# Kernel optimization log

Hardware: AMD Instinct MI355X
Metric: run time of the kernel (lower is better)

Reference implementation:

```python
import jax, jax.numpy as jnp
import numpy as np
from jax import lax

R = 7                      # pooler_resolution
SCALES = (0.25, 0.125, 0.0625, 0.03125)
SCORE_THRESH = 0.05        # args.roi_test_score_thresh
NMS_THRESH = 0.5           # args.roi_nms_thresh
TOPK = 100                 # args.roi_nms_topk_post
SCALE_CLAMP = float(np.log(1000.0 / 16))


def _pool_level(f, boxes, scale):
    # f: [C,H,W]; boxes: [M,4] in image coords. RoIPool approximated by
    # nearest-neighbor sample at each of the 7x7 bin centers.
    C, H, W = f.shape
    b = boxes * scale
    x1, y1, x2, y2 = b[:, 0], b[:, 1], b[:, 2], b[:, 3]
    bw = jnp.maximum(x2 - x1, 1.0) / R
    bh = jnp.maximum(y2 - y1, 1.0) / R
    cs = jnp.arange(R, dtype=b.dtype) + 0.5
    gx = x1[:, None] + cs * bw[:, None]          # [M,R]
    gy = y1[:, None] + cs * bh[:, None]          # [M,R]
    ix = jnp.clip(gx.astype(jnp.int32), 0, W - 1)
    iy = jnp.clip(gy.astype(jnp.int32), 0, H - 1)
    fh = jnp.transpose(f, (1, 2, 0))             # [H,W,C]
    out = fh[iy[:, :, None], ix[:, None, :]]     # [M,R,R,C]
    return jnp.transpose(out, (0, 3, 1, 2))      # [M,C,R,R]


def _assign_levels(boxes):
    # detectron2-style FPN level assignment: canonical level 4 at size 224
    w = boxes[:, 2] - boxes[:, 0]
    h = boxes[:, 3] - boxes[:, 1]
    s = jnp.sqrt(jnp.maximum(w * h, 1e-6))
    lvl = jnp.floor(4.0 + jnp.log2(s / 224.0 + 1e-8))
    return jnp.clip(lvl, 2, 5).astype(jnp.int32) - 2   # index into p2..p5


def _pool_image(f2, f3, f4, f5, boxes):
    pooled = jnp.stack([_pool_level(f, boxes, s)
                        for f, s in zip((f2, f3, f4, f5), SCALES)])  # [4,M,C,R,R]
    idx = _assign_levels(boxes)
    return pooled[idx, jnp.arange(boxes.shape[0])]     # [M,C,R,R]


def _apply_deltas(boxes, deltas):
    w = boxes[:, 2] - boxes[:, 0]
    h = boxes[:, 3] - boxes[:, 1]
    cx = boxes[:, 0] + 0.5 * w
    cy = boxes[:, 1] + 0.5 * h
    dx, dy = deltas[:, 0], deltas[:, 1]
    dw = jnp.minimum(deltas[:, 2], SCALE_CLAMP)
    dh = jnp.minimum(deltas[:, 3], SCALE_CLAMP)
    pcx = dx * w + cx
    pcy = dy * h + cy
    pw = jnp.exp(dw) * w
    ph = jnp.exp(dh) * h
    return jnp.stack([pcx - 0.5 * pw, pcy - 0.5 * ph,
                      pcx + 0.5 * pw, pcy + 0.5 * ph], axis=1)


def _pairwise_iou(a, b):
    area_a = (a[:, 2] - a[:, 0]) * (a[:, 3] - a[:, 1])
    area_b = (b[:, 2] - b[:, 0]) * (b[:, 3] - b[:, 1])
    lt = jnp.maximum(a[:, None, :2], b[None, :, :2])
    rb = jnp.minimum(a[:, None, 2:], b[None, :, 2:])
    wh = jnp.clip(rb - lt, 0.0)
    inter = wh[..., 0] * wh[..., 1]
    return inter / jnp.maximum(area_a[:, None] + area_b[None, :] - inter, 1e-9)


def _nms_image(boxes, scores, hw):
    # boxes [M,4], scores [M], hw = (H,W) float
    H, W = hw[0], hw[1]
    boxes = jnp.stack([jnp.clip(boxes[:, 0], 0.0, W),
                       jnp.clip(boxes[:, 1], 0.0, H),
                       jnp.clip(boxes[:, 2], 0.0, W),
                       jnp.clip(boxes[:, 3], 0.0, H)], axis=1)
    order = jnp.argsort(-scores)
    b = boxes[order]
    s = scores[order]
    M = b.shape[0]
    keep0 = s > SCORE_THRESH
    iou = _pairwise_iou(b, b)
    idx = jnp.arange(M)

    def body(i, keep):
        suppress = (iou[i] > NMS_THRESH) & (idx > i) & keep[i]
        return keep & ~suppress

    keep = lax.fori_loop(0, M, body, keep0)
    keep = keep & (jnp.cumsum(keep.astype(jnp.int32)) <= TOPK)
    return b, s, keep, order


def setup_inputs() -> dict:
    key = jax.random.key(0)
    ks = jax.random.split(key, 12)
    N, M, C = 2, 1000, 256
    H, W = 800, 1216
    fc_in, fc_dim = C * R * R, 1024
    p2 = jax.random.normal(ks[0], (N, C, H // 4, W // 4), jnp.float32)
    p3 = jax.random.normal(ks[1], (N, C, H // 8, W // 8), jnp.float32)
    p4 = jax.random.normal(ks[2], (N, C, H // 16, W // 16), jnp.float32)
    p5 = jax.random.normal(ks[3], (N, C, H // 32, W // 32), jnp.float32)
    u = jax.random.uniform(ks[4], (N, M, 4))
    cx = u[..., 0] * (W - 1)
    cy = u[..., 1] * (H - 1)
    bw = 16.0 + u[..., 2] * 480.0
    bh = 16.0 + u[..., 3] * 480.0
    x1 = jnp.clip(cx - 0.5 * bw, 0.0, W - 8.0)
    y1 = jnp.clip(cy - 0.5 * bh, 0.0, H - 8.0)
    x2 = jnp.clip(cx + 0.5 * bw, x1 + 4.0, float(W))
    y2 = jnp.clip(cy + 0.5 * bh, y1 + 4.0, float(H))
    proposals = jnp.stack([x1, y1, x2, y2], axis=-1)
    image_sizes = jnp.array([[H, W], [H, W]], dtype=jnp.int32)
    return {
        'p2': p2, 'p3': p3, 'p4': p4, 'p5': p5,
        'proposals': proposals, 'image_sizes': image_sizes,
        'W1': jax.random.normal(ks[5], (fc_in, fc_dim), jnp.float32) * 0.01,
        'b1': jnp.zeros((fc_dim,), jnp.float32),
        'W2': jax.random.normal(ks[6], (fc_dim, fc_dim), jnp.float32) * 0.01,
        'b2': jnp.zeros((fc_dim,), jnp.float32),
        'Wc': jax.random.normal(ks[7], (fc_dim, 2), jnp.float32) * 0.01,
        'bc': jnp.zeros((2,), jnp.float32),
        'Wb': jax.random.normal(ks[8], (fc_dim, 4), jnp.float32) * 0.001,
        'bb': jnp.zeros((4,), jnp.float32),
    }


def reference(p2, p3, p4, p5, proposals, image_sizes,
              W1, b1, W2, b2, Wc, bc, Wb, bb):
    N, M, _ = proposals.shape
    pooled = jax.vmap(_pool_image)(p2, p3, p4, p5, proposals)  # [N,M,C,R,R]
    x = pooled.reshape(N * M, -1)
    x = jax.nn.relu(x @ W1 + b1)
    x = jax.nn.relu(x @ W2 + b2)
    cls_score = x @ Wc + bc                                    # [NM,2]
    deltas = x @ Wb + bb                                       # [NM,4]
    scores = jax.nn.softmax(cls_score, axis=1)[:, 1].reshape(N, M)
    pred_boxes = _apply_deltas(proposals.reshape(-1, 4), deltas).reshape(N, M, 4)
    boxes_s, scores_s, keep, order = jax.vmap(_nms_image)(
        pred_boxes, scores, image_sizes.astype(jnp.float32))
    return boxes_s, scores_s, keep, order
```

## Files before the change

### kernel.cpp

```cpp
#include <hip/hip_runtime.h>
#include <math.h>

#define NBOX 1000
#define NIMG 2
#define CCH 256
#define FCIN 12544
#define FCD 1024
#define TOPK 100
#define SCALE_CLAMP_F ((float)4.135166556742356)
#define KC 384
#define NPANEL 33
#define RB 16
#define NGROUP 125
#define CHUNK 128
#define R1 8

__global__ void prep_kernel(const float* __restrict__ props, int* __restrict__ prep) {
    int b = blockIdx.x * blockDim.x + threadIdx.x;
    if (b >= NIMG * NBOX) return;
    int n = b / NBOX;
    const float* pr = props + (size_t)b * 4;
    float x1 = pr[0], y1 = pr[1], x2 = pr[2], y2 = pr[3];

    float w = __fsub_rn(x2, x1), h = __fsub_rn(y2, y1);
    float s = sqrtf(fmaxf(__fmul_rn(w, h), 1e-6f));
    float l2 = (float)log2((double)__fadd_rn(__fdiv_rn(s, 224.0f), 1e-8f));
    float lv = floorf(__fadd_rn(4.0f, l2));
    lv = fminf(fmaxf(lv, 2.0f), 5.0f);
    int lvl = (int)lv - 2;

    int H, W; float scale;
    if (lvl == 0)      { H = 200; W = 304; scale = 0.25f; }
    else if (lvl == 1) { H = 100; W = 152; scale = 0.125f; }
    else if (lvl == 2) { H = 50;  W = 76;  scale = 0.0625f; }
    else               { H = 25;  W = 38;  scale = 0.03125f; }

    float xs1 = __fmul_rn(x1, scale), ys1 = __fmul_rn(y1, scale);
    float xs2 = __fmul_rn(x2, scale), ys2 = __fmul_rn(y2, scale);
    float bw = __fdiv_rn(fmaxf(__fsub_rn(xs2, xs1), 1.0f), 7.0f);
    float bh = __fdiv_rn(fmaxf(__fsub_rn(ys2, ys1), 1.0f), 7.0f);

    int* pb = prep + b * 20;
    pb[0] = lvl;
    pb[1] = n * CCH * H * W;
    pb[2] = H * W;
#pragma unroll
    for (int i = 0; i < 7; i++) {
        float cs = (float)i + 0.5f;
        float gx = __fadd_rn(xs1, __fmul_rn(cs, bw));
        float gy = __fadd_rn(ys1, __fmul_rn(cs, bh));
        int vx = (int)gx;
        int vy = (int)gy;
        vx = vx < 0 ? 0 : (vx > W - 1 ? W - 1 : vx);
        vy = vy < 0 ? 0 : (vy > H - 1 ? H - 1 : vy);
        pb[4 + i] = vx;
        pb[12 + i] = vy * W;
    }
}

#define FMASTEP(KB, WV)                                               \
    {                                                                 \
        const float4* xv = (const float4*)&xs[(KB)][0];               \
        float4 a0 = xv[0], a1 = xv[1], a2 = xv[2], a3 = xv[3];        \
        float xr[16] = {a0.x, a0.y, a0.z, a0.w, a1.x, a1.y, a1.z, a1.w, \
                        a2.x, a2.y, a2.z, a2.w, a3.x, a3.y, a3.z, a3.w}; \
        _Pragma("unroll")                                             \
        for (int r = 0; r < RB; r++) {                                \
            acc[r][0] = fmaf(xr[r], WV.x, acc[r][0]);                 \
            acc[r][1] = fmaf(xr[r], WV.y, acc[r][1]);                 \
            acc[r][2] = fmaf(xr[r], WV.z, acc[r][2]);                 \
            acc[r][3] = fmaf(xr[r], WV.w, acc[r][3]);                 \
        }                                                             \
    }

__global__ __launch_bounds__(256, 4) void fc1_panel(
    const float* __restrict__ p2, const float* __restrict__ p3,
    const float* __restrict__ p4, const float* __restrict__ p5,
    const int* __restrict__ prep, const float* __restrict__ W1,
    float* __restrict__ part, int g0, int gs) {
    __shared__ float xs[CHUNK][RB];
    __shared__ int s_ix[RB][7], s_iyW[RB][7], s_HW[RB];
    __shared__ const float* s_fp[RB];

    int tid = threadIdx.x;
    int gy = blockIdx.x;
    int p = blockIdx.y;
    int row0 = (g0 + gy) * RB;
    int k0 = p * KC;
    int kt = (p == NPANEL - 1) ? 256 : KC;

    if (tid < RB) {
        const int* pb = prep + (row0 + tid) * 20;
        int lvl = pb[0];
        s_fp[tid] = (lvl == 0 ? p2 : lvl == 1 ? p3 : lvl == 2 ? p4 : p5) + pb[1];
        s_HW[tid] = pb[2];
#pragma unroll
        for (int j = 0; j < 7; j++) { s_ix[tid][j] = pb[4 + j]; s_iyW[tid][j] = pb[12 + j]; }
    }
    __syncthreads();

    float acc[RB][4];
#pragma unroll
    for (int r = 0; r < RB; r++)
#pragma unroll
        for (int j = 0; j < 4; j++) acc[r][j] = 0.0f;

    const float* wp = W1 + (size_t)k0 * FCD + tid * 4;

    for (int ck = 0; ck < kt; ck += CHUNK) {
        for (int e = tid; e < CHUNK * RB; e += 256) {
            int kk = e >> 4;
            int r = e & 15;
            int k = k0 + ck + kk;
            int c = k / 49;
            int pp = k - c * 49;
            int gyy = pp / 7;
            int gxx = pp - gyy * 7;
            xs[kk][r] = s_fp[r][c * s_HW[r] + s_iyW[r][gyy] + s_ix[r][gxx]];
        }
        __syncthreads();

        const float* wc = wp + (size_t)ck * FCD;
        float4 wA = *(const float4*)wc;
        for (int kk = 0; kk < CHUNK; kk += 2) {
            float4 wB = *(const float4*)(wc + (size_t)(kk + 1) * FCD);
            FMASTEP(kk, wA)
            if (kk + 2 < CHUNK) wA = *(const float4*)(wc + (size_t)(kk + 2) * FCD);
            FMASTEP(kk + 1, wB)
        }
        __syncthreads();
    }

    size_t pstride = (size_t)gs * RB * FCD;
    float* po = part + (size_t)p * pstride + ((size_t)gy * RB) * FCD + tid * 4;
#pragma unroll
    for (int r = 0; r < RB; r++) {
        float4 v = make_float4(acc[r][0], acc[r][1], acc[r][2], acc[r][3]);
        *(float4*)(po + (size_t)r * FCD) = v;
    }
}

__global__ void fc1_fold(const float* __restrict__ part, const float* __restrict__ b1,
                         float* __restrict__ X1, int row_base, int rows_s) {
    int idx = blockIdx.x * 256 + threadIdx.x;
    if (idx >= rows_s * FCD) return;
    size_t stride = (size_t)rows_s * FCD;
    float tot = part[idx];
    for (int p = 1; p < NPANEL; p++)
        tot = __fadd_rn(tot, part[(size_t)p * stride + idx]);
    int c = idx & (FCD - 1);
    float v = __fadd_rn(tot, b1[c]);
    X1[(size_t)row_base * FCD + idx] = fmaxf(v, 0.0f);
}

#define FMA8(BUF, KB)                                                                   \
    _Pragma("unroll")                                                                   \
    for (int u = 0; u < 8; u++) {                                                       \
        const float4* xv = (const float4*)&xs[(KB) + u][0];                             \
        float4 a0 = xv[0], a1 = xv[1];                                                  \
        float wx = BUF[u].x, wy = BUF[u].y;                                             \
        acc[0][0] = fmaf(a0.x, wx, acc[0][0]); acc[0][1] = fmaf(a0.x, wy, acc[0][1]);   \
        acc[1][0] = fmaf(a0.y, wx, acc[1][0]); acc[1][1] = fmaf(a0.y, wy, acc[1][1]);   \
        acc[2][0] = fmaf(a0.z, wx, acc[2][0]); acc[2][1] = fmaf(a0.z, wy, acc[2][1]);   \
        acc[3][0] = fmaf(a0.w, wx, acc[3][0]); acc[3][1] = fmaf(a0.w, wy, acc[3][1]);   \
        acc[4][0] = fmaf(a1.x, wx, acc[4][0]); acc[4][1] = fmaf(a1.x, wy, acc[4][1]);   \
        acc[5][0] = fmaf(a1.y, wx, acc[5][0]); acc[5][1] = fmaf(a1.y, wy, acc[5][1]);   \
        acc[6][0] = fmaf(a1.z, wx, acc[6][0]); acc[6][1] = fmaf(a1.z, wy, acc[6][1]);   \
        acc[7][0] = fmaf(a1.w, wx, acc[7][0]); acc[7][1] = fmaf(a1.w, wy, acc[7][1]);   \
    }

template <int KT>
__device__ __forceinline__ void fc_panel2(const float* __restrict__ wp,
                                          const float (*xs)[R1],
                                          float acc[R1][2]) {
    float2 wa[8], wb[8];
#pragma unroll
    for (int u = 0; u < 8; u++) wa[u] = *(const float2*)(wp + (size_t)u * FCD);
    for (int kk = 0; kk < KT; kk += 16) {
#pragma unroll
        for (int u = 0; u < 8; u++)
            wb[u] = *(const float2*)(wp + (size_t)(kk + 8 + u) * FCD);
        FMA8(wa, kk)
        if (kk + 16 < KT) {
#pragma unroll
            for (int u = 0; u < 8; u++)
                wa[u] = *(const float2*)(wp + (size_t)(kk + 16 + u) * FCD);
        }
        FMA8(wb, kk + 8)
    }
}

__global__ __launch_bounds__(256) void fc1_fallback(
    const float* __restrict__ p2, const float* __restrict__ p3,
    const float* __restrict__ p4, const float* __restrict__ p5,
    const int* __restrict__ prep, const float* __restrict__ W1,
    const float* __restrict__ b1, float* __restrict__ X1) {
    __shared__ float xs[KC][R1];
    __shared__ int s_ix[R1][7], s_iyW[R1][7], s_HW[R1];
    __shared__ const float* s_fp[R1];

    int tid = threadIdx.x;
    int c0 = blockIdx.x * 512 + tid * 2;
    int row0 = blockIdx.y * R1;

    if (tid < R1) {
        const int* pb = prep + (row0 + tid) * 20;
        int lvl = pb[0];
        s_fp[tid] = (lvl == 0 ? p2 : lvl == 1 ? p3 : lvl == 2 ? p4 : p5) + pb[1];
        s_HW[tid] = pb[2];
#pragma unroll
        for (int j = 0; j < 7; j++) { s_ix[tid][j] = pb[4 + j]; s_iyW[tid][j] = pb[12 + j]; }
    }

    float tot[R1][2];
#pragma unroll
    for (int r = 0; r < R1; r++) { tot[r][0] = 0.0f; tot[r][1] = 0.0f; }

    for (int k0 = 0; k0 < FCIN; k0 += KC) {
        int kt = FCIN - k0; if (kt > KC) kt = KC;
        __syncthreads();
        for (int e = tid; e < kt * R1; e += 256) {
            int kk = e >> 3;
            int r = e & 7;
            int k = k0 + kk;
            int c = k / 49;
            int p = k - c * 49;
            int gy = p / 7;
            int gx = p - gy * 7;
            xs[kk][r] = s_fp[r][c * s_HW[r] + s_iyW[r][gy] + s_ix[r][gx]];
        }
        __syncthreads();

        float acc[R1][2];
#pragma unroll
        for (int r = 0; r < R1; r++) { acc[r][0] = 0.0f; acc[r][1] = 0.0f; }

        const float* wp = W1 + (size_t)k0 * FCD + c0;
        if (kt == KC) fc_panel2<KC>(wp, xs, acc);
        else          fc_panel2<256>(wp, xs, acc);

#pragma unroll
        for (int r = 0; r < R1; r++) {
            tot[r][0] = __fadd_rn(tot[r][0], acc[r][0]);
            tot[r][1] = __fadd_rn(tot[r][1], acc[r][1]);
        }
    }
    float bv0 = b1[c0], bv1 = b1[c0 + 1];
#pragma unroll
    for (int r = 0; r < R1; r++) {
        float v0 = __fadd_rn(tot[r][0], bv0);
        float v1 = __fadd_rn(tot[r][1], bv1);
        X1[(size_t)(row0 + r) * FCD + c0]     = fmaxf(v0, 0.0f);
        X1[(size_t)(row0 + r) * FCD + c0 + 1] = fmaxf(v1, 0.0f);
    }
}

__global__ __launch_bounds__(256) void fc2_seq(
    const float* __restrict__ X1, const float* __restrict__ W2,
    const float* __restrict__ b2, float* __restrict__ X2) {
    __shared__ float xs[KC][R1];
    int tid = threadIdx.x;
    int c0 = blockIdx.x * 512 + tid * 2;
    int row0 = blockIdx.y * R1;

    float tot[R1][2];
#pragma unroll
    for (int r = 0; r < R1; r++) { tot[r][0] = 0.0f; tot[r][1] = 0.0f; }

    for (int k0 = 0; k0 < FCD; k0 += KC) {
        int kt = FCD - k0; if (kt > KC) kt = KC;
        __syncthreads();
        for (int e = tid; e < kt * R1; e += 256) {
            int kk = e >> 3;
            int r = e & 7;
            xs[kk][r] = X1[(size_t)(row0 + r) * FCD + k0 + kk];
        }
        __syncthreads();

        float acc[R1][2];
#pragma unroll
        for (int r = 0; r < R1; r++) { acc[r][0] = 0.0f; acc[r][1] = 0.0f; }

        const float* wp = W2 + (size_t)k0 * FCD + c0;
        if (kt == KC) fc_panel2<KC>(wp, xs, acc);
        else          fc_panel2<256>(wp, xs, acc);

#pragma unroll
        for (int r = 0; r < R1; r++) {
            tot[r][0] = __fadd_rn(tot[r][0], acc[r][0]);
            tot[r][1] = __fadd_rn(tot[r][1], acc[r][1]);
        }
    }
    float bv0 = b2[c0], bv1 = b2[c0 + 1];
#pragma unroll
    for (int r = 0; r < R1; r++) {
        float v0 = __fadd_rn(tot[r][0], bv0);
        float v1 = __fadd_rn(tot[r][1], bv1);
        X2[(size_t)(row0 + r) * FCD + c0]     = fmaxf(v0, 0.0f);
        X2[(size_t)(row0 + r) * FCD + c0 + 1] = fmaxf(v1, 0.0f);
    }
}

__global__ __launch_bounds__(256) void heads_seq(
    const float* __restrict__ X2,
    const float* __restrict__ Wc, const float* __restrict__ bc,
    const float* __restrict__ Wb, const float* __restrict__ bb_,
    const float* __restrict__ props, const int* __restrict__ img_sz,
    float* __restrict__ SC, float* __restrict__ BX) {
    int b = blockIdx.x;
    int tid = threadIdx.x;
    __shared__ float xsh[FCD];
    __shared__ float lg[6];
    for (int k = tid; k < FCD; k += 256) xsh[k] = X2[(size_t)b * FCD + k];
    __syncthreads();

    if (tid < 6) {
        const float* wp; int st; float bias;
        if (tid < 2) { wp = Wc + tid; st = 2; bias = bc[tid]; }
        else         { wp = Wb + (tid - 2); st = 4; bias = bb_[tid - 2]; }
        float tot = 0.0f;
        for (int k0 = 0; k0 < FCD; k0 += KC) {
            int kt = FCD - k0; if (kt > KC) kt = KC;
            float acc = 0.0f;
            for (int k = k0; k < k0 + kt; k++) acc = fmaf(xsh[k], wp[(size_t)k * st], acc);
            tot = __fadd_rn(tot, acc);
        }
        lg[tid] = __fadd_rn(tot, bias);
    }
    __syncthreads();

    if (tid == 0) {
        float c0 = lg[0], c1 = lg[1];
        float mx = fmaxf(c0, c1);
        float e0 = (float)exp((double)__fsub_rn(c0, mx));
        float e1 = (float)exp((double)__fsub_rn(c1, mx));
        SC[b] = __fdiv_rn(e1, __fadd_rn(e0, e1));

        int n = b / NBOX;
        const float* pr = props + (size_t)b * 4;
        float x1 = pr[0], y1 = pr[1], x2 = pr[2], y2 = pr[3];
        float w = __fsub_rn(x2, x1), h = __fsub_rn(y2, y1);
        float cx = __fadd_rn(x1, __fmul_rn(0.5f, w));
        float cy = __fadd_rn(y1, __fmul_rn(0.5f, h));
        float dx = lg[2], dy = lg[3];
        float dw = fminf(lg[4], SCALE_CLAMP_F);
        float dh = fminf(lg[5], SCALE_CLAMP_F);
        float pcx = __fadd_rn(__fmul_rn(dx, w), cx);
        float pcy = __fadd_rn(__fmul_rn(dy, h), cy);
        float pw = __fmul_rn((float)exp((double)dw), w);
        float ph = __fmul_rn((float)exp((double)dh), h);
        float bx1 = __fsub_rn(pcx, __fmul_rn(0.5f, pw));
        float by1 = __fsub_rn(pcy, __fmul_rn(0.5f, ph));
        float bx2 = __fadd_rn(pcx, __fmul_rn(0.5f, pw));
        float by2 = __fadd_rn(pcy, __fmul_rn(0.5f, ph));
        float Hf = (float)img_sz[n * 2 + 0], Wf = (float)img_sz[n * 2 + 1];
        bx1 = fminf(fmaxf(bx1, 0.0f), Wf);
        by1 = fminf(fmaxf(by1, 0.0f), Hf);
        bx2 = fminf(fmaxf(bx2, 0.0f), Wf);
        by2 = fminf(fmaxf(by2, 0.0f), Hf);
        BX[(size_t)b * 4 + 0] = bx1;
        BX[(size_t)b * 4 + 1] = by1;
        BX[(size_t)b * 4 + 2] = bx2;
        BX[(size_t)b * 4 + 3] = by2;
    }
}

__global__ __launch_bounds__(1024) void nms_kernel(const float* __restrict__ SC,
                                                   const float* __restrict__ BX,
                                                   float* __restrict__ out) {
    int n = blockIdx.x;
    __shared__ float sraw[NBOX];
    __shared__ float ssort[NBOX];
    __shared__ float bsort[NBOX][4];
    __shared__ int ord[NBOX];
    __shared__ unsigned char keep[NBOX];
    int tid = threadIdx.x;

    for (int j = tid; j < NBOX; j += 1024) sraw[j] = SC[n * NBOX + j];
    __syncthreads();

    if (tid < NBOX) {
        float sj = sraw[tid];
        int r = 0;
        for (int k = 0; k < NBOX; k++) {
            float sk = sraw[k];
            r += (sk > sj) || (sk == sj && k < tid);
        }
        ord[r] = tid;
        ssort[r] = sj;
#pragma unroll
        for (int k = 0; k < 4; k++) bsort[r][k] = BX[((size_t)n * NBOX + tid) * 4 + k];
        keep[r] = (sj > 0.05f) ? 1 : 0;
    }
    __syncthreads();

    for (int i = 0; i < NBOX - 1; i++) {
        if (keep[i] && tid > i && tid < NBOX && keep[tid]) {
            float ax1 = bsort[i][0], ay1 = bsort[i][1], ax2 = bsort[i][2], ay2 = bsort[i][3];
            float bx1 = bsort[tid][0], by1 = bsort[tid][1], bx2 = bsort[tid][2], by2 = bsort[tid][3];
            float areaA = __fmul_rn(__fsub_rn(ax2, ax1), __fsub_rn(ay2, ay1));
            float areaB = __fmul_rn(__fsub_rn(bx2, bx1), __fsub_rn(by2, by1));
            float ix1 = fmaxf(ax1, bx1), iy1 = fmaxf(ay1, by1);
            float ix2 = fminf(ax2, bx2), iy2 = fminf(ay2, by2);
            float iw = fmaxf(__fsub_rn(ix2, ix1), 0.0f);
            float ih = fmaxf(__fsub_rn(iy2, iy1), 0.0f);
            float inter = __fmul_rn(iw, ih);
            float denom = fmaxf(__fsub_rn(__fadd_rn(areaA, areaB), inter), 1e-9f);
            if (__fdiv_rn(inter, denom) > 0.5f) keep[tid] = 0;
        }
        __syncthreads();
    }

    if (tid == 0) {
        int c = 0;
        for (int r = 0; r < NBOX; r++) {
            int k = keep[r];
            c += k;
            keep[r] = (k && (c <= TOPK)) ? 1 : 0;
        }
    }
    __syncthreads();

    float* boxes_o = out;
    float* scores_o = out + (size_t)NIMG * NBOX * 4;
    float* keep_o = scores_o + (size_t)NIMG * NBOX;
    float* ord_o = keep_o + (size_t)NIMG * NBOX;
    for (int r = tid; r < NBOX; r += 1024) {
#pragma unroll
        for (int k = 0; k < 4; k++)
            boxes_o[((size_t)n * NBOX + r) * 4 + k] = bsort[r][k];
        scores_o[n * NBOX + r] = ssort[r];
        keep_o[n * NBOX + r] = (float)keep[r];
        ord_o[n * NBOX + r] = (float)ord[r];
    }
}

extern "C" void kernel_launch(void* const* d_in, const int* in_sizes, int n_in,
                              void* d_out, int out_size, void* d_ws, size_t ws_size,
                              hipStream_t stream) {
    const float* p2 = (const float*)d_in[0];
    const float* p3 = (const float*)d_in[1];
    const float* p4 = (const float*)d_in[2];
    const float* p5 = (const float*)d_in[3];
    const float* props = (const float*)d_in[4];
    const int* img = (const int*)d_in[5];
    const float* W1 = (const float*)d_in[6];
    const float* b1 = (const float*)d_in[7];
    const float* W2 = (const float*)d_in[8];
    const float* b2 = (const float*)d_in[9];
    const float* Wc = (const float*)d_in[10];
    const float* bc = (const float*)d_in[11];
    const float* Wb = (const float*)d_in[12];
    const float* bb = (const float*)d_in[13];

    float* X1 = (float*)d_ws;
    float* X2 = X1 + (size_t)2000 * FCD;
    float* SCf = X2 + (size_t)2000 * FCD;
    float* BXf = SCf + 2000;
    int* prep = (int*)(BXf + 8000);
    float* part = (float*)(prep + 2000 * 20);
    size_t used = (size_t)((char*)part - (char*)d_ws);
    size_t avail = ws_size > used ? ws_size - used : 0;

    prep_kernel<<<(NIMG * NBOX + 255) / 256, 256, 0, stream>>>(props, prep);

    int gmax = 0;
    const int cand[4] = {125, 63, 32, 16};
    for (int i = 0; i < 4; i++) {
        size_t need = (size_t)NPANEL * cand[i] * RB * FCD * sizeof(float);
        if (need <= avail) { gmax = cand[i]; break; }
    }

    if (gmax > 0) {
        for (int g0 = 0; g0 < NGROUP; g0 += gmax) {
            int gs = NGROUP - g0; if (gs > gmax) gs = gmax;
            dim3 gA(gs, NPANEL);
            fc1_panel<<<gA, 256, 0, stream>>>(p2, p3, p4, p5, prep, W1, part, g0, gs);
            int rows_s = gs * RB;
            int nelem = rows_s * FCD;
            fc1_fold<<<(nelem + 255) / 256, 256, 0, stream>>>(part, b1, X1, g0 * RB, rows_s);
        }
    } else {
        dim3 gfc(2, (NIMG * NBOX) / R1);
        fc1_fallback<<<gfc, 256, 0, stream>>>(p2, p3, p4, p5, prep, W1, b1, X1);
    }

    dim3 gfc2(2, (NIMG * NBOX) / R1);
    fc2_seq<<<gfc2, 256, 0, stream>>>(X1, W2, b2, X2);

    heads_seq<<<NIMG * NBOX, 256, 0, stream>>>(X2, Wc, bc, Wb, bb, props, img, SCf, BXf);

    nms_kernel<<<NIMG, 1024, 0, stream>>>(SCf, BXf, (float*)d_out);
}
```

Measured before the change: 1.177 ms.

## Split FC2 GEMM into K-panels with partial sums and separate fold

Replaces the sequential fc2 kernel with a split-K panel kernel that computes 8-row by 1024-column tiles over three K panels into a workspace, followed by a generic fold kernel that sums panels, adds bias and applies ReLU. The fc1 fold kernel is generalised to take the panel count, and the FC1 FMA macro is manually unrolled. This raises parallelism and register-tiled reuse for the second FC layer, at the cost of extra workspace traffic and one more launch. It falls back to the old kernel when the workspace is too small, and the split-K summation order may change rounding relative to the sequential path.

```diff
diff --git a/kernel.cpp b/kernel.cpp
--- a/kernel.cpp
+++ b/kernel.cpp
@@ -13,6 +13,8 @@
 #define RB 16
 #define NGROUP 125
 #define CHUNK 128
+#define RB2 8
+#define NP2 3
 #define R1 8
 
 __global__ void prep_kernel(const float* __restrict__ props, int* __restrict__ prep) {
@@ -58,19 +60,21 @@
     }
 }
 
-#define FMASTEP(KB, WV)                                               \
+#define FR4(AX, RI)                                       \
+    acc[RI][0] = fmaf(AX, WV.x, acc[RI][0]);              \
+    acc[RI][1] = fmaf(AX, WV.y, acc[RI][1]);              \
+    acc[RI][2] = fmaf(AX, WV.z, acc[RI][2]);              \
+    acc[RI][3] = fmaf(AX, WV.w, acc[RI][3]);
+
+#define FMASTEP(KB, WVAL)                                             \
     {                                                                 \
         const float4* xv = (const float4*)&xs[(KB)][0];               \
         float4 a0 = xv[0], a1 = xv[1], a2 = xv[2], a3 = xv[3];        \
-        float xr[16] = {a0.x, a0.y, a0.z, a0.w, a1.x, a1.y, a1.z, a1.w, \
-                        a2.x, a2.y, a2.z, a2.w, a3.x, a3.y, a3.z, a3.w}; \
-        _Pragma("unroll")                                             \
-        for (int r = 0; r < RB; r++) {                                \
-            acc[r][0] = fmaf(xr[r], WV.x, acc[r][0]);                 \
-            acc[r][1] = fmaf(xr[r], WV.y, acc[r][1]);                 \
-            acc[r][2] = fmaf(xr[r], WV.z, acc[r][2]);                 \
-            acc[r][3] = fmaf(xr[r], WV.w, acc[r][3]);                 \
-        }                                                             \
+        float4 WV = WVAL;                                             \
+        FR4(a0.x, 0)  FR4(a0.y, 1)  FR4(a0.z, 2)  FR4(a0.w, 3)       \
+        FR4(a1.x, 4)  FR4(a1.y, 5)  FR4(a1.z, 6)  FR4(a1.w, 7)       \
+        FR4(a2.x, 8)  FR4(a2.y, 9)  FR4(a2.z, 10) FR4(a2.w, 11)      \
+        FR4(a3.x, 12) FR4(a3.y, 13) FR4(a3.z, 14) FR4(a3.w, 15)      \
     }
 
 __global__ __launch_bounds__(256, 4) void fc1_panel(
@@ -140,17 +144,110 @@
     }
 }
 
-__global__ void fc1_fold(const float* __restrict__ part, const float* __restrict__ b1,
-                         float* __restrict__ X1, int row_base, int rows_s) {
+__global__ __launch_bounds__(256, 4) void fc2_panel(
+    const float* __restrict__ X1, const float* __restrict__ W2,
+    float* __restrict__ part) {
+    __shared__ float xs2[CHUNK][RB2];
+    int tid = threadIdx.x;
+    int gy = blockIdx.x;
+    int p = blockIdx.y;
+    int row0 = gy * RB2;
+    int k0 = p * KC;
+    int kt = (p == NP2 - 1) ? 256 : KC;
+
+    float acc[RB2][4];
+#pragma unroll
+    for (int r = 0; r < RB2; r++)
+#pragma unroll
+        for (int j = 0; j < 4; j++) acc[r][j] = 0.0f;
+
+    const float* wp = W2 + (size_t)k0 * FCD + tid * 4;
+
+    for (int ck = 0; ck < kt; ck += CHUNK) {
+        for (int e = tid; e < CHUNK * RB2; e += 256) {
+            int kk = e >> 3;
+            int r = e & 7;
+            xs2[kk][r] = X1[(size_t)(row0 + r) * FCD + k0 + ck + kk];
+        }
+        __syncthreads();
+
+        const float* wc = wp + (size_t)ck * FCD;
+        float4 wA = *(const float4*)wc;
+        for (int kk = 0; kk < CHUNK; kk += 2) {
+            float4 wB = *(const float4*)(wc + (size_t)(kk + 1) * FCD);
+            {
+                const float4* xv = (const float4*)&xs2[kk][0];
+                float4 a0 = xv[0], a1 = xv[1];
+                float4 WV = wA;
+#pragma unroll
+                for (int j = 0; j < 1; j++) {
+                    acc[0][0] = fmaf(a0.x, WV.x, acc[0][0]); acc[0][1] = fmaf(a0.x, WV.y, acc[0][1]);
+                    acc[0][2] = fmaf(a0.x, WV.z, acc[0][2]); acc[0][3] = fmaf(a0.x, WV.w, acc[0][3]);
+                    acc[1][0] = fmaf(a0.y, WV.x, acc[1][0]); acc[1][1] = fmaf(a0.y, WV.y, acc[1][1]);
+                    acc[1][2] = fmaf(a0.y, WV.z, acc[1][2]); acc[1][3] = fmaf(a0.y, WV.w, acc[1][3]);
+                    acc[2][0] = fmaf(a0.z, WV.x, acc[2][0]); acc[2][1] = fmaf(a0.z, WV.y, acc[2][1]);
+                    acc[2][2] = fmaf(a0.z, WV.z, acc[2][2]); acc[2][3] = fmaf(a0.z, WV.w, acc[2][3]);
+                    acc[3][0] = fmaf(a0.w, WV.x, acc[3][0]); acc[3][1] = fmaf(a0.w, WV.y, acc[3][1]);
+                    acc[3][2] = fmaf(a0.w, WV.z, acc[3][2]); acc[3][3] = fmaf(a0.w, WV.w, acc[3][3]);
+                    acc[4][0] = fmaf(a1.x, WV.x, acc[4][0]); acc[4][1] = fmaf(a1.x, WV.y, acc[4][1]);
+                    acc[4][2] = fmaf(a1.x, WV.z, acc[4][2]); acc[4][3] = fmaf(a1.x, WV.w, acc[4][3]);
+                    acc[5][0] = fmaf(a1.y, WV.x, acc[5][0]); acc[5][1] = fmaf(a1.y, WV.y, acc[5][1]);
+                    acc[5][2] = fmaf(a1.y, WV.z, acc[5][2]); acc[5][3] = fmaf(a1.y, WV.w, acc[5][3]);
+                    acc[6][0] = fmaf(a1.z, WV.x, acc[6][0]); acc[6][1] = fmaf(a1.z, WV.y, acc[6][1]);
+                    acc[6][2] = fmaf(a1.z, WV.z, acc[6][2]); acc[6][3] = fmaf(a1.z, WV.w, acc[6][3]);
+                    acc[7][0] = fmaf(a1.w, WV.x, acc[7][0]); acc[7][1] = fmaf(a1.w, WV.y, acc[7][1]);
+                    acc[7][2] = fmaf(a1.w, WV.z, acc[7][2]); acc[7][3] = fmaf(a1.w, WV.w, acc[7][3]);
+                }
+            }
+            if (kk + 2 < CHUNK) wA = *(const float4*)(wc + (size_t)(kk + 2) * FCD);
+            {
+                const float4* xv = (const float4*)&xs2[kk + 1][0];
+                float4 a0 = xv[0], a1 = xv[1];
+                float4 WV = wB;
+#pragma unroll
+                for (int j = 0; j < 1; j++) {
+                    acc[0][0] = fmaf(a0.x, WV.x, acc[0][0]); acc[0][1] = fmaf(a0.x, WV.y, acc[0][1]);
+                    acc[0][2] = fmaf(a0.x, WV.z, acc[0][2]); acc[0][3] = fmaf(a0.x, WV.w, acc[0][3]);
+                    acc[1][0] = fmaf(a0.y, WV.x, acc[1][0]); acc[1][1] = fmaf(a0.y, WV.y, acc[1][1]);
+                    acc[1][2] = fmaf(a0.y, WV.z, acc[1][2]); acc[1][3] = fmaf(a0.y, WV.w, acc[1][3]);
+                    acc[2][0] = fmaf(a0.z, WV.x, acc[2][0]); acc[2][1] = fmaf(a0.z, WV.y, acc[2][1]);
+                    acc[2][2] = fmaf(a0.z, WV.z, acc[2][2]); acc[2][3] = fmaf(a0.z, WV.w, acc[2][3]);
+                    acc[3][0] = fmaf(a0.w, WV.x, acc[3][0]); acc[3][1] = fmaf(a0.w, WV.y, acc[3][1]);
+                    acc[3][2] = fmaf(a0.w, WV.z, acc[3][2]); acc[3][3] = fmaf(a0.w, WV.w, acc[3][3]);
+                    acc[4][0] = fmaf(a1.x, WV.x, acc[4][0]); acc[4][1] = fmaf(a1.x, WV.y, acc[4][1]);
+                    acc[4][2] = fmaf(a1.x, WV.z, acc[4][2]); acc[4][3] = fmaf(a1.x, WV.w, acc[4][3]);
+                    acc[5][0] = fmaf(a1.y, WV.x, acc[5][0]); acc[5][1] = fmaf(a1.y, WV.y, acc[5][1]);
+                    acc[5][2] = fmaf(a1.y, WV.z, acc[5][2]); acc[5][3] = fmaf(a1.y, WV.w, acc[5][3]);
+                    acc[6][0] = fmaf(a1.z, WV.x, acc[6][0]); acc[6][1] = fmaf(a1.z, WV.y, acc[6][1]);
+                    acc[6][2] = fmaf(a1.z, WV.z, acc[6][2]); acc[6][3] = fmaf(a1.z, WV.w, acc[6][3]);
+                    acc[7][0] = fmaf(a1.w, WV.x, acc[7][0]); acc[7][1] = fmaf(a1.w, WV.y, acc[7][1]);
+                    acc[7][2] = fmaf(a1.w, WV.z, acc[7][2]); acc[7][3] = fmaf(a1.w, WV.w, acc[7][3]);
+                }
+            }
+        }
+        __syncthreads();
+    }
+
+    size_t pstride = (size_t)NIMG * NBOX * FCD;
+    float* po = part + (size_t)p * pstride + ((size_t)row0) * FCD + tid * 4;
+#pragma unroll
+    for (int r = 0; r < RB2; r++) {
+        float4 v = make_float4(acc[r][0], acc[r][1], acc[r][2], acc[r][3]);
+        *(float4*)(po + (size_t)r * FCD) = v;
+    }
+}
+
+__global__ void fold_bias_relu(const float* __restrict__ part, const float* __restrict__ bias,
+                               float* __restrict__ Xout, int row_base, int rows_s, int npanel) {
     int idx = blockIdx.x * 256 + threadIdx.x;
     if (idx >= rows_s * FCD) return;
     size_t stride = (size_t)rows_s * FCD;
     float tot = part[idx];
-    for (int p = 1; p < NPANEL; p++)
+    for (int p = 1; p < npanel; p++)
         tot = __fadd_rn(tot, part[(size_t)p * stride + idx]);
     int c = idx & (FCD - 1);
-    float v = __fadd_rn(tot, b1[c]);
-    X1[(size_t)row_base * FCD + idx] = fmaxf(v, 0.0f);
+    float v = __fadd_rn(tot, bias[c]);
+    Xout[(size_t)row_base * FCD + idx] = fmaxf(v, 0.0f);
 }
 
 #define FMA8(BUF, KB)                                                                   \
@@ -476,17 +573,26 @@
             int gs = NGROUP - g0; if (gs > gmax) gs = gmax;
             dim3 gA(gs, NPANEL);
             fc1_panel<<<gA, 256, 0, stream>>>(p2, p3, p4, p5, prep, W1, part, g0, gs);
-            int rows_s = gs * RB;
-            int nelem = rows_s * FCD;
-            fc1_fold<<<(nelem + 255) / 256, 256, 0, stream>>>(part, b1, X1, g0 * RB, rows_s);
+            int nelem = gs * RB * FCD;
+            fold_bias_relu<<<(nelem + 255) / 256, 256, 0, stream>>>(part, b1, X1,
+                                                                    g0 * RB, gs * RB, NPANEL);
         }
     } else {
         dim3 gfc(2, (NIMG * NBOX) / R1);
         fc1_fallback<<<gfc, 256, 0, stream>>>(p2, p3, p4, p5, prep, W1, b1, X1);
     }
 
-    dim3 gfc2(2, (NIMG * NBOX) / R1);
-    fc2_seq<<<gfc2, 256, 0, stream>>>(X1, W2, b2, X2);
+    size_t need2 = (size_t)NP2 * NIMG * NBOX * FCD * sizeof(float);
+    if (need2 <= avail) {
+        dim3 g2(NIMG * NBOX / RB2, NP2);
+        fc2_panel<<<g2, 256, 0, stream>>>(X1, W2, part);
+        int nelem2 = NIMG * NBOX * FCD;
+        fold_bias_relu<<<(nelem2 + 255) / 256, 256, 0, stream>>>(part, b2, X2,
+                                                                 0, NIMG * NBOX, NP2);
+    } else {
+        dim3 gfc2(2, (NIMG * NBOX) / R1);
+        fc2_seq<<<gfc2, 256, 0, stream>>>(X1, W2, b2, X2);
+    }
 
     heads_seq<<<NIMG * NBOX, 256, 0, stream>>>(X2, Wc, bc, Wb, bb, props, img, SCf, BXf);
 
```

After: 1.195 ms. No clear change (+1.5%).
